# Kernel optimization log

Hardware: AMD Instinct MI355X
Metric: run time of the kernel (lower is better)

Reference implementation:

```python
import jax, jax.numpy as jnp
import numpy as np

B, A, H, DKEY, NMEM = 1024, 4, 512, 512, 65536
OBS, E1, E2 = 9, 64, 128
DIN = E2 + A + 1  # 133


def _lin_init(k, out_d, in_d):
    s = 1.0 / np.sqrt(in_d)
    kw, kb = jax.random.split(k)
    w = jax.random.uniform(kw, (out_d, in_d), jnp.float32, -s, s)
    b = jax.random.uniform(kb, (out_d,), jnp.float32, -s, s)
    return w, b


def setup_inputs() -> dict:
    key = jax.random.key(0)
    ks = jax.random.split(key, 16)
    inp = {}
    inp["obs"] = jax.random.normal(ks[0], (B, OBS), jnp.float32)
    inp["p_action"] = jax.random.uniform(ks[1], (B, A), jnp.float32)
    inp["p_reward"] = jax.random.normal(ks[2], (B, 1), jnp.float32)
    inp["h0"] = jnp.zeros((1, B, H), jnp.float32)
    inp["c0"] = jnp.zeros((1, B, H), jnp.float32)
    inp["cue"] = jax.random.normal(ks[3], (B, DKEY), jnp.float32)
    # encoder params
    inp["enc_w1"], inp["enc_b1"] = _lin_init(ks[4], E1, OBS)
    inp["enc_w2"], inp["enc_b2"] = _lin_init(ks[5], E2, E1)
    # episodic LSTM params (5 gates: i, f, g, o, r)
    s = 1.0 / np.sqrt(H)
    inp["w_ih"] = jax.random.uniform(ks[6], (5 * H, DIN), jnp.float32, -s, s)
    inp["w_hh"] = jax.random.uniform(ks[7], (5 * H, H), jnp.float32, -s, s)
    inp["b_ih"] = jax.random.uniform(ks[8], (5 * H,), jnp.float32, -s, s)
    inp["b_hh"] = jax.random.uniform(ks[9], (5 * H,), jnp.float32, -s, s)
    # actor / critic heads
    inp["actor_w"], inp["actor_b"] = _lin_init(ks[10], A, H)
    inp["critic_w"], inp["critic_b"] = _lin_init(ks[11], 1, H)
    # DND memory store (keys / values)
    inp["dnd_keys"] = jax.random.normal(ks[12], (NMEM, DKEY), jnp.float32)
    inp["dnd_vals"] = jax.random.normal(ks[13], (NMEM, H), jnp.float32) * 0.1
    return inp


def reference(obs, p_action, p_reward, h0, c0, cue,
              enc_w1, enc_b1, enc_w2, enc_b2,
              w_ih, w_hh, b_ih, b_hh,
              actor_w, actor_b, critic_w, critic_b,
              dnd_keys, dnd_vals):
    # --- encoder MLP ---
    feats = jax.nn.relu(jax.nn.relu(obs @ enc_w1.T + enc_b1) @ enc_w2.T + enc_b2)  # [B, 128]
    x_t = jnp.concatenate([feats, p_action, p_reward], axis=-1)  # [B, DIN]

    # --- DND retrieval: l2 kernel -> softmax-weighted sum of values ---
    d2 = (jnp.sum(cue * cue, axis=-1, keepdims=True)
          - 2.0 * (cue @ dnd_keys.T)
          + jnp.sum(dnd_keys * dnd_keys, axis=-1))  # [B, NMEM]
    sims = -jnp.sqrt(jnp.maximum(d2, 1e-12))
    w = jax.nn.softmax(sims, axis=-1)
    m_t = w @ dnd_vals  # [B, H]

    # --- episodic LSTM step (single timestep) ---
    h, c = h0[0], c0[0]  # [B, H]
    z = x_t @ w_ih.T + h @ w_hh.T + b_ih + b_hh  # [B, 5H]
    i_g = jax.nn.sigmoid(z[:, 0 * H:1 * H])
    f_g = jax.nn.sigmoid(z[:, 1 * H:2 * H])
    g_g = jnp.tanh(z[:, 2 * H:3 * H])
    o_g = jax.nn.sigmoid(z[:, 3 * H:4 * H])
    r_g = jax.nn.sigmoid(z[:, 4 * H:5 * H])  # reinstatement gate for memory
    c_new = f_g * c + i_g * g_g + r_g * m_t
    h_new = o_g * jnp.tanh(c_new)

    # --- heads ---
    action_logits = h_new @ actor_w.T + actor_b  # [B, A]
    value_estimate = h_new @ critic_w.T + critic_b  # [B, 1]
    return action_logits, value_estimate, h_new[None], c_new[None], feats
```

## Files before the change

### kernel.cpp

```cpp
#include <hip/hip_runtime.h>

typedef __bf16 bf16x8 __attribute__((ext_vector_type(8)));
typedef float  f32x4  __attribute__((ext_vector_type(4)));

#define NMEM_   65536
#define NCHUNK_ 16
#define NKC_    (NMEM_/NCHUNK_)
#define XPD_    160

#define WS_KB    ((size_t)0)
#define WS_VT    ((size_t)67108864)
#define WS_KNRM  ((size_t)134217728)
#define WS_QB    ((size_t)134479872)
#define WS_QQ    ((size_t)135528448)
#define WS_OP    ((size_t)135532544)
#define WS_LP    ((size_t)169086976)
#define WS_MT    ((size_t)169152512)
#define WS_XP    ((size_t)171249664)
#define WS_HB    ((size_t)171577344)
#define WS_WIHP  ((size_t)172625920)
#define WS_WHHB  ((size_t)173445120)
#define WS_Z     ((size_t)176066560)

#define OUT_LOG   0
#define OUT_VAL   4096
#define OUT_H     5120
#define OUT_C     529408
#define OUT_FEATS 1053696

__device__ __forceinline__ void gload16(const void* g, void* l) {
    __builtin_amdgcn_global_load_lds(
        (const __attribute__((address_space(1))) void*)g,
        (__attribute__((address_space(3))) void*)l, 16, 0, 0);
}

__global__ __launch_bounds__(256) void enc_kernel(
    const float* __restrict__ obs, const float* __restrict__ pa, const float* __restrict__ pr,
    const float* __restrict__ w1, const float* __restrict__ b1,
    const float* __restrict__ w2, const float* __restrict__ b2,
    float* __restrict__ feats_out, __bf16* __restrict__ xp)
{
    __shared__ float W1s[64*9];
    __shared__ float B1s[64];
    __shared__ float W2s[128*64];
    __shared__ float B2s[128];
    int t = threadIdx.x;
    for (int i = t; i < 64*9;   i += 256) W1s[i] = w1[i];
    for (int i = t; i < 64;     i += 256) B1s[i] = b1[i];
    for (int i = t; i < 128*64; i += 256) W2s[i] = w2[i];
    for (int i = t; i < 128;    i += 256) B2s[i] = b2[i];
    __syncthreads();
    int row = blockIdx.x * 256 + t;
    float ob[9];
    #pragma unroll
    for (int j = 0; j < 9; j++) ob[j] = obs[row*9 + j];
    float h1[64];
    #pragma unroll 4
    for (int i = 0; i < 64; i++) {
        float a = B1s[i];
        #pragma unroll
        for (int j = 0; j < 9; j++) a += ob[j] * W1s[i*9 + j];
        h1[i] = fmaxf(a, 0.f);
    }
    for (int j = 0; j < 128; j += 4) {
        float a0 = B2s[j], a1 = B2s[j+1], a2 = B2s[j+2], a3 = B2s[j+3];
        for (int i = 0; i < 64; i++) {
            float h = h1[i];
            a0 += h * W2s[(j+0)*64 + i];
            a1 += h * W2s[(j+1)*64 + i];
            a2 += h * W2s[(j+2)*64 + i];
            a3 += h * W2s[(j+3)*64 + i];
        }
        a0 = fmaxf(a0,0.f); a1 = fmaxf(a1,0.f); a2 = fmaxf(a2,0.f); a3 = fmaxf(a3,0.f);
        feats_out[row*128 + j+0] = a0; feats_out[row*128 + j+1] = a1;
        feats_out[row*128 + j+2] = a2; feats_out[row*128 + j+3] = a3;
        xp[row*XPD_ + j+0] = (__bf16)a0; xp[row*XPD_ + j+1] = (__bf16)a1;
        xp[row*XPD_ + j+2] = (__bf16)a2; xp[row*XPD_ + j+3] = (__bf16)a3;
    }
    #pragma unroll
    for (int k = 0; k < 4; k++) xp[row*XPD_ + 128 + k] = (__bf16)pa[row*4 + k];
    xp[row*XPD_ + 132] = (__bf16)pr[row];
    #pragma unroll
    for (int c = 133; c < 160; c++) xp[row*XPD_ + c] = (__bf16)0.f;
}

#define CV_KEYS 16384
#define CV_CUE  (CV_KEYS + 256)
#define CV_VT   (CV_CUE + 8192)
#define CM_N1 (2560*512)
#define CM_N2 (1024*512)
#define CM_N3 (2560*160)
#define CV_ALL  (CV_VT + (CM_N1 + CM_N2 + CM_N3 + 255)/256)

__global__ __launch_bounds__(256) void conv_all(
    const float* __restrict__ keys, const float* __restrict__ cue,
    const float* __restrict__ vals,
    const float* __restrict__ whh, const float* __restrict__ h0,
    const float* __restrict__ wih,
    __bf16* __restrict__ Kb, float* __restrict__ knrm,
    __bf16* __restrict__ Qb, float* __restrict__ qq,
    __bf16* __restrict__ Vt,
    __bf16* __restrict__ Whhb, __bf16* __restrict__ Hb, __bf16* __restrict__ Wihp)
{
    int bid = blockIdx.x;
    if (bid < CV_CUE) {
        const float* src; __bf16* dst; float* nrm; int swz, rbase;
        if (bid < CV_KEYS) { src = keys; dst = Kb; nrm = knrm; swz = 1; rbase = bid*4; }
        else               { src = cue;  dst = Qb; nrm = qq;  swz = 0; rbase = (bid-CV_KEYS)*4; }
        int row  = rbase + (threadIdx.x >> 6);
        int lane = threadIdx.x & 63;
        const float* s = src + (size_t)row * 512 + lane * 8;
        float4 v0 = *(const float4*)s;
        float4 v1 = *(const float4*)(s + 4);
        float ss = v0.x*v0.x + v0.y*v0.y + v0.z*v0.z + v0.w*v0.w
                 + v1.x*v1.x + v1.y*v1.y + v1.z*v1.z + v1.w*v1.w;
        bf16x8 o;
        o[0]=(__bf16)v0.x; o[1]=(__bf16)v0.y; o[2]=(__bf16)v0.z; o[3]=(__bf16)v0.w;
        o[4]=(__bf16)v1.x; o[5]=(__bf16)v1.y; o[6]=(__bf16)v1.z; o[7]=(__bf16)v1.w;
        int xorv = swz ? ((row & 15) << 4) : 0;
        *(bf16x8*)((char*)dst + (size_t)row * 1024 + ((lane * 16) ^ xorv)) = o;
        #pragma unroll
        for (int m = 1; m < 64; m <<= 1) ss += __shfl_xor(ss, m, 64);
        if (lane == 0) nrm[row] = ss;
        return;
    }
    if (bid < CV_VT) {
        __shared__ float Ls[64*65];
        int local = bid - CV_CUE;
        int k0 = (local & 1023) * 64, d0 = (local >> 10) * 64;
        int rr = threadIdx.x >> 6, cc = threadIdx.x & 63;
        #pragma unroll
        for (int i = 0; i < 16; i++) {
            int row = i*4 + rr;
            Ls[row*65 + cc] = vals[(size_t)(k0 + row) * 512 + d0 + cc];
        }
        __syncthreads();
        #pragma unroll
        for (int i = 0; i < 16; i++) {
            int drow = i*4 + rr;
            Vt[(size_t)(d0 + drow) * 65536 + k0 + cc] = (__bf16)Ls[cc*65 + drow];
        }
        return;
    }
    {
        int i = (bid - CV_VT) * 256 + threadIdx.x;
        if (i < CM_N1) { Whhb[i] = (__bf16)whh[i]; return; }
        i -= CM_N1;
        if (i < CM_N2) { Hb[i] = (__bf16)h0[i]; return; }
        i -= CM_N2;
        if (i < CM_N3) {
            int r = i / 160, c = i - r * 160;
            Wihp[i] = (c < 133) ? (__bf16)wih[r*133 + c] : (__bf16)0.f;
        }
    }
}

__global__ __launch_bounds__(512) void flash_kernel(
    const __bf16* __restrict__ Kb, const __bf16* __restrict__ Vt,
    const __bf16* __restrict__ Qb, const float* __restrict__ qq,
    const float* __restrict__ knrm,
    float* __restrict__ Opart, float* __restrict__ Lpart)
{
    extern __shared__ char smem[];
    char*  KL  = smem;
    char*  Plb = smem + 131072;
    float* Lb  = (float*)(smem + 147456);

    const int tid = threadIdx.x, lane = tid & 63, w = tid >> 6;
    const int wq = w >> 1, wk = w & 1;
    const int lr = lane & 15, lq = lane >> 4;
    const int chunk = blockIdx.x & 15, qt = blockIdx.x >> 4;
    const int q0 = qt * 64, key0 = chunk * NKC_;

    bf16x8 qA[16];
    #pragma unroll
    for (int ks = 0; ks < 16; ks++)
        qA[ks] = *(const bf16x8*)(Qb + (size_t)(q0 + wq*16 + lr)*512 + ks*32 + lq*8);
    float qq4[4];
    #pragma unroll
    for (int r = 0; r < 4; r++)
        qq4[r] = qq[q0 + wq*16 + lq*4 + r];

    const float*  knp  = knrm + key0 + wk*32 + lr;
    const __bf16* vrow = Vt + (size_t)(w*64 + lr)*65536 + key0 + lq*8;
    const char*   kg   = (const char*)Kb + (size_t)key0 * 1024;

    #pragma unroll
    for (int r = 0; r < 8; ++r)
        gload16(kg + r*8192 + w*1024 + lane*16, KL + r*8192 + w*1024);
    asm volatile("s_waitcnt vmcnt(0)" ::: "memory");
    __builtin_amdgcn_s_barrier();

    f32x4 oacc[4][4] = {};
    float lsum[4] = {};
    int cur = 0;

    #pragma unroll 1
    for (int t = 0; t < 64; ++t) {
        float kn0 = knp[t*64];
        float kn1 = knp[t*64 + 16];
        const __bf16* vb = vrow + ((t + 63) & 63) * 64;
        bf16x8 vf[2][4];
        #pragma unroll
        for (int k2 = 0; k2 < 2; ++k2)
            #pragma unroll
            for (int mf = 0; mf < 4; ++mf)
                vf[k2][mf] = *(const bf16x8*)(vb + k2*32 + (size_t)mf*1048576);
        {
            const char* src = kg + (size_t)((t+1)&63)*65536;
            char* dst = KL + (cur^1)*65536;
            #pragma unroll
            for (int r = 0; r < 8; ++r)
                gload16(src + r*8192 + w*1024 + lane*16, dst + r*8192 + w*1024);
        }
        asm volatile("s_waitcnt vmcnt(18) lgkmcnt(0)" ::: "memory");
        __builtin_amdgcn_sched_barrier(0);
        __builtin_amdgcn_s_barrier();
        const char* kl = KL + cur*65536 + (wk*32 + lr)*1024;
        f32x4 s0 = {0.f,0.f,0.f,0.f}, s1 = {0.f,0.f,0.f,0.f};
        __builtin_amdgcn_s_setprio(1);
        #pragma unroll
        for (int ks = 0; ks < 16; ++ks) {
            int off = (ks*64 + lq*16) ^ (lr << 4);
            bf16x8 kf0 = *(const bf16x8*)(kl + off);
            bf16x8 kf1 = *(const bf16x8*)(kl + 16384 + off);
            s0 = __builtin_amdgcn_mfma_f32_16x16x32_bf16(qA[ks], kf0, s0, 0, 0, 0);
            s1 = __builtin_amdgcn_mfma_f32_16x16x32_bf16(qA[ks], kf1, s1, 0, 0, 0);
        }
        if (t) {
            const char* pb_ = Plb + ((t+1)&1)*8192;
            #pragma unroll
            for (int k2 = 0; k2 < 2; ++k2)
                #pragma unroll
                for (int f2 = 0; f2 < 4; ++f2) {
                    bf16x8 pf = *(const bf16x8*)(pb_ + (f2*16 + lr)*128
                                 + ((k2*64 + lq*16) ^ ((lr & 7) << 4)));
                    #pragma unroll
                    for (int mf = 0; mf < 4; ++mf)
                        oacc[mf][f2] = __builtin_amdgcn_mfma_f32_16x16x32_bf16(
                            vf[k2][mf], pf, oacc[mf][f2], 0, 0, 0);
                }
        }
        __builtin_amdgcn_s_setprio(0);
        char* pw = Plb + (t&1)*8192;
        #pragma unroll
        for (int r = 0; r < 4; ++r) {
            float d20 = fmaxf(qq4[r] + kn0 - 2.f*s0[r], 1e-12f);
            float d21 = fmaxf(qq4[r] + kn1 - 2.f*s1[r], 1e-12f);
            float p0 = __expf(-__builtin_amdgcn_sqrtf(d20));
            float p1 = __expf(-__builtin_amdgcn_sqrtf(d21));
            lsum[r] += p0 + p1;
            int row_ = wq*16 + lq*4 + r;
            int sw = (row_ & 7) << 4;
            *(__bf16*)(pw + row_*128 + (((wk*32 + lr)*2     ) ^ sw)) = (__bf16)p0;
            *(__bf16*)(pw + row_*128 + (((wk*32 + lr)*2 + 32) ^ sw)) = (__bf16)p1;
        }
        cur ^= 1;
    }

    {
        const __bf16* vb = vrow + 63*64;
        bf16x8 vf[2][4];
        #pragma unroll
        for (int k2 = 0; k2 < 2; ++k2)
            #pragma unroll
            for (int mf = 0; mf < 4; ++mf)
                vf[k2][mf] = *(const bf16x8*)(vb + k2*32 + (size_t)mf*1048576);
        asm volatile("s_waitcnt lgkmcnt(0)" ::: "memory");
        __builtin_amdgcn_sched_barrier(0);
        __builtin_amdgcn_s_barrier();
        const char* pb_ = Plb + 8192;
        #pragma unroll
        for (int k2 = 0; k2 < 2; ++k2)
            #pragma unroll
            for (int f2 = 0; f2 < 4; ++f2) {
                bf16x8 pf = *(const bf16x8*)(pb_ + (f2*16 + lr)*128
                             + ((k2*64 + lq*16) ^ ((lr & 7) << 4)));
                #pragma unroll
                for (int mf = 0; mf < 4; ++mf)
                    oacc[mf][f2] = __builtin_amdgcn_mfma_f32_16x16x32_bf16(
                        vf[k2][mf], pf, oacc[mf][f2], 0, 0, 0);
            }
    }
    asm volatile("s_waitcnt vmcnt(0)" ::: "memory");

    const size_t obase = (size_t)((chunk*16 + qt)*512) * 64;
    #pragma unroll
    for (int mf = 0; mf < 4; ++mf)
        #pragma unroll
        for (int f2 = 0; f2 < 4; ++f2)
            #pragma unroll
            for (int r = 0; r < 4; ++r) {
                int d = w*64 + mf*16 + lq*4 + r;
                Opart[obase + (size_t)d*64 + f2*16 + lr] = oacc[mf][f2][r];
            }
    #pragma unroll
    for (int r = 0; r < 4; ++r) {
        float s = lsum[r];
        s += __shfl_xor(s, 1, 64); s += __shfl_xor(s, 2, 64);
        s += __shfl_xor(s, 4, 64); s += __shfl_xor(s, 8, 64);
        if (lr == 0) Lb[(wq*16 + lq*4 + r)*2 + wk] = s;
    }
    __syncthreads();
    if (tid < 64)
        Lpart[chunk*1024 + q0 + tid] = Lb[tid*2] + Lb[tid*2 + 1];
}

__global__ __launch_bounds__(256) void combine_kernel(
    const float* __restrict__ Opart, const float* __restrict__ Lpart,
    float* __restrict__ mt)
{
    __shared__ float Ts[64*65];
    __shared__ float Ls[64];
    int qt = blockIdx.x, db = blockIdx.y * 64, t = threadIdx.x;
    float acc[16] = {};
    for (int c = 0; c < NCHUNK_; c++) {
        size_t base = (size_t)((c*16 + qt)*512 + db) * 64;
        #pragma unroll
        for (int i = 0; i < 16; i++) acc[i] += Opart[base + t + 256*i];
    }
    if (t < 64) {
        float s = 0.f;
        for (int c = 0; c < NCHUNK_; c++) s += Lpart[c*1024 + qt*64 + t];
        Ls[t] = 1.f / s;
    }
    #pragma unroll
    for (int i = 0; i < 16; i++) {
        int idx = t + 256*i;
        Ts[(idx >> 6)*65 + (idx & 63)] = acc[i];
    }
    __syncthreads();
    #pragma unroll
    for (int i = 0; i < 16; i++) {
        int widx = t + 256*i;
        int dloc = widx & 63, ql = widx >> 6;
        mt[(size_t)(qt*64 + ql)*512 + db + dloc] = Ts[dloc*65 + ql] * Ls[ql];
    }
}

__global__ __launch_bounds__(256) void lstm_gemm(
    const __bf16* __restrict__ X,  const __bf16* __restrict__ Wx,
    const __bf16* __restrict__ Hb, const __bf16* __restrict__ Wh,
    const float* __restrict__ bi,  const float* __restrict__ bh,
    float* __restrict__ z)
{
    int tid = threadIdx.x, lane = tid & 63, w = tid >> 6;
    int wr = w >> 1, wc = w & 1;
    int lr = lane & 15, lq = lane >> 4;
    int q0 = blockIdx.x * 64, n0 = blockIdx.y * 64;
    f32x4 acc00 = {}, acc01 = {}, acc10 = {}, acc11 = {};
    #pragma unroll
    for (int ks = 0; ks < 5; ks++) {
        bf16x8 a0 = *(const bf16x8*)(X  + (size_t)(q0 + wr*32      + lr)*XPD_ + ks*32 + lq*8);
        bf16x8 a1 = *(const bf16x8*)(X  + (size_t)(q0 + wr*32 + 16 + lr)*XPD_ + ks*32 + lq*8);
        bf16x8 b0 = *(const bf16x8*)(Wx + (size_t)(n0 + wc*32      + lr)*XPD_ + ks*32 + lq*8);
        bf16x8 b1 = *(const bf16x8*)(Wx + (size_t)(n0 + wc*32 + 16 + lr)*XPD_ + ks*32 + lq*8);
        acc00 = __builtin_amdgcn_mfma_f32_16x16x32_bf16(a0, b0, acc00, 0,0,0);
        acc01 = __builtin_amdgcn_mfma_f32_16x16x32_bf16(a0, b1, acc01, 0,0,0);
        acc10 = __builtin_amdgcn_mfma_f32_16x16x32_bf16(a1, b0, acc10, 0,0,0);
        acc11 = __builtin_amdgcn_mfma_f32_16x16x32_bf16(a1, b1, acc11, 0,0,0);
    }
    #pragma unroll
    for (int ks = 0; ks < 16; ks++) {
        bf16x8 a0 = *(const bf16x8*)(Hb + (size_t)(q0 + wr*32      + lr)*512 + ks*32 + lq*8);
        bf16x8 a1 = *(const bf16x8*)(Hb + (size_t)(q0 + wr*32 + 16 + lr)*512 + ks*32 + lq*8);
        bf16x8 b0 = *(const bf16x8*)(Wh + (size_t)(n0 + wc*32      + lr)*512 + ks*32 + lq*8);
        bf16x8 b1 = *(const bf16x8*)(Wh + (size_t)(n0 + wc*32 + 16 + lr)*512 + ks*32 + lq*8);
        acc00 = __builtin_amdgcn_mfma_f32_16x16x32_bf16(a0, b0, acc00, 0,0,0);
        acc01 = __builtin_amdgcn_mfma_f32_16x16x32_bf16(a0, b1, acc01, 0,0,0);
        acc10 = __builtin_amdgcn_mfma_f32_16x16x32_bf16(a1, b0, acc10, 0,0,0);
        acc11 = __builtin_amdgcn_mfma_f32_16x16x32_bf16(a1, b1, acc11, 0,0,0);
    }
    int nA = n0 + wc*32 + lr, nB = nA + 16;
    float biasA = bi[nA] + bh[nA], biasB = bi[nB] + bh[nB];
    #pragma unroll
    for (int r = 0; r < 4; r++) {
        int qa = q0 + wr*32 + lq*4 + r, qb = qa + 16;
        z[(size_t)qa*2560 + nA] = acc00[r] + biasA;
        z[(size_t)qa*2560 + nB] = acc01[r] + biasB;
        z[(size_t)qb*2560 + nA] = acc10[r] + biasA;
        z[(size_t)qb*2560 + nB] = acc11[r] + biasB;
    }
}

__global__ __launch_bounds__(256) void gates_kernel(
    const float* __restrict__ z,  const float* __restrict__ c0, const float* __restrict__ mt,
    const float* __restrict__ aw, const float* __restrict__ ab,
    const float* __restrict__ cw, const float* __restrict__ cb,
    float* __restrict__ out)
{
    __shared__ float hrow[512];
    __shared__ float red[256];
    int q = blockIdx.x, t = threadIdx.x;
    const float* zq = z + (size_t)q * 2560;
    for (int d = t; d < 512; d += 256) {
        float zi = zq[d], zf = zq[512 + d], zg = zq[1024 + d], zo = zq[1536 + d], zr = zq[2048 + d];
        float ig = 1.f / (1.f + __expf(-zi));
        float fg = 1.f / (1.f + __expf(-zf));
        float gg = tanhf(zg);
        float og = 1.f / (1.f + __expf(-zo));
        float rg = 1.f / (1.f + __expf(-zr));
        float cn = fg * c0[(size_t)q*512 + d] + ig * gg + rg * mt[(size_t)q*512 + d];
        float hn = og * tanhf(cn);
        out[OUT_H + (size_t)q*512 + d] = hn;
        out[OUT_C + (size_t)q*512 + d] = cn;
        hrow[d] = hn;
    }
    __syncthreads();
    for (int o = 0; o < 5; o++) {
        const float* wv = (o < 4) ? (aw + o*512) : cw;
        float p = 0.f;
        for (int d = t; d < 512; d += 256) p += hrow[d] * wv[d];
        red[t] = p;
        __syncthreads();
        for (int s = 128; s > 0; s >>= 1) {
            if (t < s) red[t] += red[t + s];
            __syncthreads();
        }
        if (t == 0) {
            float v = red[0] + ((o < 4) ? ab[o] : cb[0]);
            if (o < 4) out[OUT_LOG + q*4 + o] = v;
            else       out[OUT_VAL + q] = v;
        }
        __syncthreads();
    }
}

extern "C" void kernel_launch(void* const* d_in, const int* in_sizes, int n_in,
                              void* d_out, int out_size, void* d_ws, size_t ws_size,
                              hipStream_t stream) {
    (void)in_sizes; (void)n_in; (void)out_size; (void)ws_size;
    const float* obs   = (const float*)d_in[0];
    const float* pa    = (const float*)d_in[1];
    const float* pr    = (const float*)d_in[2];
    const float* h0    = (const float*)d_in[3];
    const float* c0    = (const float*)d_in[4];
    const float* cue   = (const float*)d_in[5];
    const float* ew1   = (const float*)d_in[6];
    const float* eb1   = (const float*)d_in[7];
    const float* ew2   = (const float*)d_in[8];
    const float* eb2   = (const float*)d_in[9];
    const float* w_ih  = (const float*)d_in[10];
    const float* w_hh  = (const float*)d_in[11];
    const float* b_ih  = (const float*)d_in[12];
    const float* b_hh  = (const float*)d_in[13];
    const float* aw    = (const float*)d_in[14];
    const float* ab    = (const float*)d_in[15];
    const float* cw    = (const float*)d_in[16];
    const float* cb    = (const float*)d_in[17];
    const float* keys  = (const float*)d_in[18];
    const float* vals  = (const float*)d_in[19];

    char* ws = (char*)d_ws;
    __bf16* Kb    = (__bf16*)(ws + WS_KB);
    __bf16* Vt    = (__bf16*)(ws + WS_VT);
    float*  knrm  = (float*) (ws + WS_KNRM);
    __bf16* Qb    = (__bf16*)(ws + WS_QB);
    float*  qq    = (float*) (ws + WS_QQ);
    float*  Opart = (float*) (ws + WS_OP);
    float*  Lpart = (float*) (ws + WS_LP);
    float*  mt    = (float*) (ws + WS_MT);
    __bf16* Xp    = (__bf16*)(ws + WS_XP);
    __bf16* Hb    = (__bf16*)(ws + WS_HB);
    __bf16* Wihp  = (__bf16*)(ws + WS_WIHP);
    __bf16* Whhb  = (__bf16*)(ws + WS_WHHB);
    float*  zbuf  = (float*) (ws + WS_Z);
    float*  out   = (float*)d_out;

    (void)hipFuncSetAttribute((const void*)flash_kernel,
                              hipFuncAttributeMaxDynamicSharedMemorySize, 147968);

    enc_kernel<<<4, 256, 0, stream>>>(obs, pa, pr, ew1, eb1, ew2, eb2, out + OUT_FEATS, Xp);
    conv_all<<<CV_ALL, 256, 0, stream>>>(keys, cue, vals, w_hh, h0, w_ih,
                                         Kb, knrm, Qb, qq, Vt, Whhb, Hb, Wihp);
    flash_kernel<<<256, 512, 147968, stream>>>(Kb, Vt, Qb, qq, knrm, Opart, Lpart);
    combine_kernel<<<dim3(16, 8), 256, 0, stream>>>(Opart, Lpart, mt);
    lstm_gemm<<<dim3(16, 40), 256, 0, stream>>>(Xp, Wihp, Hb, Whhb, b_ih, b_hh, zbuf);
    gates_kernel<<<1024, 256, 0, stream>>>(zbuf, c0, mt, aw, ab, cw, cb, out);
}
```

Measured before the change: 395.1 us.

## Quantize DND keys and cue to FP8 for the QK score MFMA

Converts the memory keys and query cues to FP8 e4m3 instead of bf16. The score computation then uses fp8 MFMA with half the LDS footprint and global traffic for keys. The LDS buffers are resized and the load and wait counts adjusted to match. This targets key-streaming bandwidth, LDS pressure and occupancy, but trades away a lot of precision in the distance computation. That error is amplified by sqrt and softmax over 65536 keys and may break the accuracy tolerance.

```diff
diff --git a/kernel.cpp b/kernel.cpp
--- a/kernel.cpp
+++ b/kernel.cpp
@@ -1,4 +1,5 @@
 #include <hip/hip_runtime.h>
+#include <hip/hip_fp8.h>
 
 typedef __bf16 bf16x8 __attribute__((ext_vector_type(8)));
 typedef float  f32x4  __attribute__((ext_vector_type(4)));
@@ -34,6 +35,11 @@
         (__attribute__((address_space(3))) void*)l, 16, 0, 0);
 }
 
+__device__ __forceinline__ unsigned char to_fp8(float f) {
+    __hip_fp8_e4m3 v(f);
+    return *(unsigned char*)&v;
+}
+
 __global__ __launch_bounds__(256) void enc_kernel(
     const float* __restrict__ obs, const float* __restrict__ pa, const float* __restrict__ pr,
     const float* __restrict__ w1, const float* __restrict__ b1,
@@ -97,14 +103,14 @@
     const float* __restrict__ vals,
     const float* __restrict__ whh, const float* __restrict__ h0,
     const float* __restrict__ wih,
-    __bf16* __restrict__ Kb, float* __restrict__ knrm,
-    __bf16* __restrict__ Qb, float* __restrict__ qq,
+    unsigned char* __restrict__ Kb, float* __restrict__ knrm,
+    unsigned char* __restrict__ Qb, float* __restrict__ qq,
     __bf16* __restrict__ Vt,
     __bf16* __restrict__ Whhb, __bf16* __restrict__ Hb, __bf16* __restrict__ Wihp)
 {
     int bid = blockIdx.x;
     if (bid < CV_CUE) {
-        const float* src; __bf16* dst; float* nrm; int swz, rbase;
+        const float* src; unsigned char* dst; float* nrm; int swz, rbase;
         if (bid < CV_KEYS) { src = keys; dst = Kb; nrm = knrm; swz = 1; rbase = bid*4; }
         else               { src = cue;  dst = Qb; nrm = qq;  swz = 0; rbase = (bid-CV_KEYS)*4; }
         int row  = rbase + (threadIdx.x >> 6);
@@ -114,11 +120,14 @@
         float4 v1 = *(const float4*)(s + 4);
         float ss = v0.x*v0.x + v0.y*v0.y + v0.z*v0.z + v0.w*v0.w
                  + v1.x*v1.x + v1.y*v1.y + v1.z*v1.z + v1.w*v1.w;
-        bf16x8 o;
-        o[0]=(__bf16)v0.x; o[1]=(__bf16)v0.y; o[2]=(__bf16)v0.z; o[3]=(__bf16)v0.w;
-        o[4]=(__bf16)v1.x; o[5]=(__bf16)v1.y; o[6]=(__bf16)v1.z; o[7]=(__bf16)v1.w;
-        int xorv = swz ? ((row & 15) << 4) : 0;
-        *(bf16x8*)((char*)dst + (size_t)row * 1024 + ((lane * 16) ^ xorv)) = o;
+        union { unsigned char b[8]; long v; } pk;
+        pk.b[0] = to_fp8(v0.x); pk.b[1] = to_fp8(v0.y);
+        pk.b[2] = to_fp8(v0.z); pk.b[3] = to_fp8(v0.w);
+        pk.b[4] = to_fp8(v1.x); pk.b[5] = to_fp8(v1.y);
+        pk.b[6] = to_fp8(v1.z); pk.b[7] = to_fp8(v1.w);
+        int c = lane * 8;
+        int addr = swz ? (c ^ ((row & 15) << 4)) : c;
+        *(long*)(dst + (size_t)row * 512 + addr) = pk.v;
         #pragma unroll
         for (int m = 1; m < 64; m <<= 1) ss += __shfl_xor(ss, m, 64);
         if (lane == 0) nrm[row] = ss;
@@ -156,15 +165,15 @@
 }
 
 __global__ __launch_bounds__(512) void flash_kernel(
-    const __bf16* __restrict__ Kb, const __bf16* __restrict__ Vt,
-    const __bf16* __restrict__ Qb, const float* __restrict__ qq,
+    const unsigned char* __restrict__ Kb, const __bf16* __restrict__ Vt,
+    const unsigned char* __restrict__ Qb, const float* __restrict__ qq,
     const float* __restrict__ knrm,
     float* __restrict__ Opart, float* __restrict__ Lpart)
 {
     extern __shared__ char smem[];
     char*  KL  = smem;
-    char*  Plb = smem + 131072;
-    float* Lb  = (float*)(smem + 147456);
+    char*  Plb = smem + 65536;
+    float* Lb  = (float*)(smem + 81920);
 
     const int tid = threadIdx.x, lane = tid & 63, w = tid >> 6;
     const int wq = w >> 1, wk = w & 1;
@@ -172,10 +181,10 @@
     const int chunk = blockIdx.x & 15, qt = blockIdx.x >> 4;
     const int q0 = qt * 64, key0 = chunk * NKC_;
 
-    bf16x8 qA[16];
+    long qA[16];
     #pragma unroll
     for (int ks = 0; ks < 16; ks++)
-        qA[ks] = *(const bf16x8*)(Qb + (size_t)(q0 + wq*16 + lr)*512 + ks*32 + lq*8);
+        qA[ks] = *(const long*)(Qb + (size_t)(q0 + wq*16 + lr)*512 + ks*32 + lq*8);
     float qq4[4];
     #pragma unroll
     for (int r = 0; r < 4; r++)
@@ -183,17 +192,18 @@
 
     const float*  knp  = knrm + key0 + wk*32 + lr;
     const __bf16* vrow = Vt + (size_t)(w*64 + lr)*65536 + key0 + lq*8;
-    const char*   kg   = (const char*)Kb + (size_t)key0 * 1024;
-
-    #pragma unroll
-    for (int r = 0; r < 8; ++r)
-        gload16(kg + r*8192 + w*1024 + lane*16, KL + r*8192 + w*1024);
+    const char*   kg   = (const char*)Kb + (size_t)key0 * 512;
+
+    #pragma unroll
+    for (int r = 0; r < 4; ++r)
+        gload16(kg + r*8192 + tid*16, KL + r*8192 + tid*16);
     asm volatile("s_waitcnt vmcnt(0)" ::: "memory");
     __builtin_amdgcn_s_barrier();
 
     f32x4 oacc[4][4] = {};
     float lsum[4] = {};
     int cur = 0;
+    const int kxor = lr << 4;
 
     #pragma unroll 1
     for (int t = 0; t < 64; ++t) {
@@ -207,25 +217,25 @@
             for (int mf = 0; mf < 4; ++mf)
                 vf[k2][mf] = *(const bf16x8*)(vb + k2*32 + (size_t)mf*1048576);
         {
-            const char* src = kg + (size_t)((t+1)&63)*65536;
-            char* dst = KL + (cur^1)*65536;
-            #pragma unroll
-            for (int r = 0; r < 8; ++r)
-                gload16(src + r*8192 + w*1024 + lane*16, dst + r*8192 + w*1024);
-        }
-        asm volatile("s_waitcnt vmcnt(18) lgkmcnt(0)" ::: "memory");
+            const char* src = kg + (size_t)((t+1)&63)*32768;
+            char* dst = KL + (cur^1)*32768;
+            #pragma unroll
+            for (int r = 0; r < 4; ++r)
+                gload16(src + r*8192 + tid*16, dst + r*8192 + tid*16);
+        }
+        asm volatile("s_waitcnt vmcnt(14) lgkmcnt(0)" ::: "memory");
         __builtin_amdgcn_sched_barrier(0);
         __builtin_amdgcn_s_barrier();
-        const char* kl = KL + cur*65536 + (wk*32 + lr)*1024;
+        const char* kl = KL + cur*32768 + (wk*32 + lr)*512;
         f32x4 s0 = {0.f,0.f,0.f,0.f}, s1 = {0.f,0.f,0.f,0.f};
         __builtin_amdgcn_s_setprio(1);
         #pragma unroll
         for (int ks = 0; ks < 16; ++ks) {
-            int off = (ks*64 + lq*16) ^ (lr << 4);
-            bf16x8 kf0 = *(const bf16x8*)(kl + off);
-            bf16x8 kf1 = *(const bf16x8*)(kl + 16384 + off);
-            s0 = __builtin_amdgcn_mfma_f32_16x16x32_bf16(qA[ks], kf0, s0, 0, 0, 0);
-            s1 = __builtin_amdgcn_mfma_f32_16x16x32_bf16(qA[ks], kf1, s1, 0, 0, 0);
+            int off = (ks*32 + lq*8) ^ kxor;
+            long kf0 = *(const long*)(kl + off);
+            long kf1 = *(const long*)(kl + 8192 + off);
+            s0 = __builtin_amdgcn_mfma_f32_16x16x32_fp8_fp8(qA[ks], kf0, s0, 0, 0, 0);
+            s1 = __builtin_amdgcn_mfma_f32_16x16x32_fp8_fp8(qA[ks], kf1, s1, 0, 0, 0);
         }
         if (t) {
             const char* pb_ = Plb + ((t+1)&1)*8192;
@@ -452,10 +462,10 @@
     const float* vals  = (const float*)d_in[19];
 
     char* ws = (char*)d_ws;
-    __bf16* Kb    = (__bf16*)(ws + WS_KB);
+    unsigned char* Kb = (unsigned char*)(ws + WS_KB);
     __bf16* Vt    = (__bf16*)(ws + WS_VT);
     float*  knrm  = (float*) (ws + WS_KNRM);
-    __bf16* Qb    = (__bf16*)(ws + WS_QB);
+    unsigned char* Qb = (unsigned char*)(ws + WS_QB);
     float*  qq    = (float*) (ws + WS_QQ);
     float*  Opart = (float*) (ws + WS_OP);
     float*  Lpart = (float*) (ws + WS_LP);
@@ -468,12 +478,12 @@
     float*  out   = (float*)d_out;
 
     (void)hipFuncSetAttribute((const void*)flash_kernel,
-                              hipFuncAttributeMaxDynamicSharedMemorySize, 147968);
+                              hipFuncAttributeMaxDynamicSharedMemorySize, 82432);
 
     enc_kernel<<<4, 256, 0, stream>>>(obs, pa, pr, ew1, eb1, ew2, eb2, out + OUT_FEATS, Xp);
     conv_all<<<CV_ALL, 256, 0, stream>>>(keys, cue, vals, w_hh, h0, w_ih,
                                          Kb, knrm, Qb, qq, Vt, Whhb, Hb, Wihp);
-    flash_kernel<<<256, 512, 147968, stream>>>(Kb, Vt, Qb, qq, knrm, Opart, Lpart);
+    flash_kernel<<<256, 512, 82432, stream>>>(Kb, Vt, Qb, qq, knrm, Opart, Lpart);
     combine_kernel<<<dim3(16, 8), 256, 0, stream>>>(Opart, Lpart, mt);
     lstm_gemm<<<dim3(16, 40), 256, 0, stream>>>(Xp, Wihp, Hb, Whhb, b_ih, b_hh, zbuf);
     gates_kernel<<<1024, 256, 0, stream>>>(zbuf, c0, mt, aw, ab, cw, cb, out);
```

New measurement: 386.0 us. -2.3%, faster.
